# Optimization experiments

Measured on AMD Instinct MI355X. Metric: run time of the kernel, lower is better.

Reference implementation:

```python
import jax, jax.numpy as jnp
import numpy as np

NEG_SLOPE = 0.01  # nn.LeakyReLU default used in module

def leaky_relu(x):
    return jnp.where(x >= 0, x, NEG_SLOPE * x)

def setup_inputs() -> dict:
    key = jax.random.key(0)
    k1, k2, k3, k4, k5 = jax.random.split(key, 5)
    B, S, D, H, E = 4, 2048, 1024, 2048, 8
    s_in = 1.0 / np.sqrt(D)
    return {
        "inputs": jax.random.normal(k1, (B, S, D), dtype=jnp.float32),
        "Wg": jax.random.normal(k2, (E, D), dtype=jnp.float32) * s_in,
        "bg": jax.random.normal(k3, (E,), dtype=jnp.float32) * s_in,
        "We": jax.random.normal(k4, (E, H, D), dtype=jnp.float32) * s_in,
        "be": jax.random.normal(k5, (E, H), dtype=jnp.float32) * s_in,
    }

def reference(inputs, Wg, bg, We, be):
    # gate: [B,S,E]
    gate_logits = jnp.einsum('bsd,ed->bse', inputs, Wg) + bg
    gate_probs = jax.nn.softmax(gate_logits, axis=-1)
    # all experts densely: [B,S,E,H]
    expert_out = leaky_relu(jnp.einsum('bsd,ehd->bseh', inputs, We) + be)
    # gate-weighted reduction over experts: [B,S,H]
    weighted = jnp.einsum('bseh,bse->bsh', expert_out, gate_probs)
    return weighted
```

## Files before the change

kernel.cpp:

```cpp
#include <hip/hip_runtime.h>
#include <hip/hip_bf16.h>
#include <math.h>

#define M_TOK 8192
#define N_H   2048
#define K_D   1024
#define N_E   8

typedef __bf16 bf16x8 __attribute__((ext_vector_type(8)));
typedef __bf16 bf16x4 __attribute__((ext_vector_type(4)));
typedef float  f32x4  __attribute__((ext_vector_type(4)));

__device__ inline f32x4 mfma16(bf16x8 a, bf16x8 b, f32x4 c) {
  return __builtin_amdgcn_mfma_f32_16x16x32_bf16(a, b, c, 0, 0, 0);
}

__device__ inline void load16_lds(const void* g, void* l) {
  __builtin_amdgcn_global_load_lds(
      (const __attribute__((address_space(1))) void*)g,
      (__attribute__((address_space(3))) void*)l, 16, 0, 0);
}

__global__ __launch_bounds__(256) void cvt_kernel(const float* __restrict__ src,
                                                  __bf16* __restrict__ dst,
                                                  int n4) {
  int i = blockIdx.x * blockDim.x + threadIdx.x;
  const int stride = gridDim.x * blockDim.x;
  for (; i < n4; i += stride) {
    float4 v = ((const float4*)src)[i];
    bf16x4 o = {(__bf16)v.x, (__bf16)v.y, (__bf16)v.z, (__bf16)v.w};
    *(bf16x4*)(dst + (size_t)i * 4) = o;
  }
}

__global__ __launch_bounds__(256) void gate_kernel(const float* __restrict__ X,
                                                   const float* __restrict__ Wg,
                                                   const float* __restrict__ bg,
                                                   float* __restrict__ gate,
                                                   __bf16* __restrict__ Xb) {
  const int tid = threadIdx.x;
  const int lane = tid & 63;
  const int wv = tid >> 6;
  const int token = blockIdx.x * 4 + wv;
  const float* xrow = X + (size_t)token * K_D;

  float xr[16];
#pragma unroll
  for (int i = 0; i < 16; ++i) xr[i] = xrow[lane + i * 64];

#pragma unroll
  for (int i = 0; i < 16; ++i)
    Xb[(size_t)token * K_D + lane + i * 64] = (__bf16)xr[i];

  float l[N_E];
#pragma unroll
  for (int e = 0; e < N_E; ++e) {
    const float* wrow = Wg + e * K_D;
    float s = 0.f;
#pragma unroll
    for (int i = 0; i < 16; ++i) s += xr[i] * wrow[lane + i * 64];
#pragma unroll
    for (int off = 32; off > 0; off >>= 1) s += __shfl_xor(s, off);
    l[e] = s + bg[e];
  }
  float mx = l[0];
#pragma unroll
  for (int e = 1; e < N_E; ++e) mx = fmaxf(mx, l[e]);
  float p[N_E], den = 0.f;
#pragma unroll
  for (int e = 0; e < N_E; ++e) { p[e] = expf(l[e] - mx); den += p[e]; }
  const float inv = 1.f / den;
  if (lane == 0) {
#pragma unroll
    for (int e = 0; e < N_E; ++e) gate[(size_t)token * N_E + e] = p[e] * inv;
  }
}

__global__ __launch_bounds__(256, 2) void moe_main(
    const __bf16* __restrict__ Xb, const __bf16* __restrict__ Wb,
    const float* __restrict__ gate, const float* __restrict__ be,
    float* __restrict__ out) {
  __shared__ __bf16 As[2][128 * 32];
  __shared__ __bf16 Bs[2][256 * 32];
  __shared__ float gS[128 * 8];
  __shared__ float bS[8 * 128];

  const int tid = threadIdx.x;
  const int lane = tid & 63;
  const int wv = tid >> 6;
  const int wr = wv >> 1, wn = wv & 1;
  const int row0 = blockIdx.x * 128;
  const int col0 = blockIdx.y * 128;

  for (int i = tid; i < 1024; i += 256) {
    gS[i] = gate[(size_t)row0 * N_E + i];
    bS[i] = be[(size_t)(i >> 7) * N_H + col0 + (i & 127)];
  }

  const int rA = tid >> 2;
  const int kk = (tid & 3) * 8;
  const __bf16* aB = Xb + (size_t)(row0 + rA) * K_D + kk;
  const __bf16* bB = Wb + (size_t)(col0 + rA) * K_D + kk;

  const int lr = lane & 15;
  const int lk = (lane >> 4) * 8;
  const __bf16* aRd0 = &As[0][(wr * 64 + lr) * 32 + lk];
  const __bf16* aRd1 = &As[1][(wr * 64 + lr) * 32 + lk];
  const __bf16* bRd0 = &Bs[0][(wn * 64 + lr) * 32 + lk];
  const __bf16* bRd1 = &Bs[1][(wn * 64 + lr) * 32 + lk];

  f32x4 fin[4][4];
#pragma unroll
  for (int m = 0; m < 4; ++m)
#pragma unroll
    for (int h = 0; h < 4; ++h) fin[m][h] = (f32x4){0.f, 0.f, 0.f, 0.f};

  f32x4 acc[4][8];
#pragma unroll
  for (int m = 0; m < 4; ++m)
#pragma unroll
    for (int n = 0; n < 8; ++n) acc[m][n] = (f32x4){0.f, 0.f, 0.f, 0.f};

  auto STAGE = [&](int tn, int bufN) {
    const int k0 = (tn & 31) << 5;
    const size_t pOff = (size_t)(tn >> 5) << 22;
    const __bf16* a = aB + k0;
    load16_lds(a, &As[bufN][wv * 512]);
    load16_lds(a + (size_t)64 * K_D, &As[bufN][2048 + wv * 512]);
    const __bf16* b = bB + pOff + k0;
    load16_lds(b, &Bs[bufN][wv * 512]);
    load16_lds(b + (size_t)64 * K_D, &Bs[bufN][2048 + wv * 512]);
    load16_lds(b + (size_t)N_H * K_D, &Bs[bufN][4096 + wv * 512]);
    load16_lds(b + (size_t)(N_H + 64) * K_D, &Bs[bufN][6144 + wv * 512]);
  };

  auto EPI = [&](int p) {
    const int e0 = p * 2;
#pragma unroll
    for (int m = 0; m < 4; ++m) {
#pragma unroll
      for (int j = 0; j < 4; ++j) {
        const int r = wr * 64 + m * 16 + (lane >> 4) * 4 + j;
        const float g0 = gS[r * 8 + e0];
        const float g1 = gS[r * 8 + e0 + 1];
#pragma unroll
        for (int h = 0; h < 4; ++h) {
          const int c = wn * 64 + h * 16 + lr;
          float v0 = acc[m][h][j] + bS[e0 * 128 + c];
          v0 = (v0 >= 0.f) ? v0 : 0.01f * v0;
          float v1 = acc[m][4 + h][j] + bS[(e0 + 1) * 128 + c];
          v1 = (v1 >= 0.f) ? v1 : 0.01f * v1;
          fin[m][h][j] += g0 * v0 + g1 * v1;
        }
      }
    }
#pragma unroll
    for (int m = 0; m < 4; ++m)
#pragma unroll
      for (int n = 0; n < 8; ++n) acc[m][n] = (f32x4){0.f, 0.f, 0.f, 0.f};
  };

  auto STEP = [&](int t, const __bf16* aRd, const __bf16* bRd, int nextBuf) {
    if (t < 127) STAGE(t + 1, nextBuf);
    bf16x8 af[4];
#pragma unroll
    for (int m = 0; m < 4; ++m) af[m] = *(const bf16x8*)(aRd + m * 512);
    __builtin_amdgcn_s_setprio(1);
#pragma unroll
    for (int n = 0; n < 8; ++n) {
      const bf16x8 bfr =
          *(const bf16x8*)(bRd + ((n >> 2) * 128 + (n & 3) * 16) * 32);
#pragma unroll
      for (int m = 0; m < 4; ++m)
        acc[m][n] = mfma16(af[m], bfr, acc[m][n]);
    }
    __builtin_amdgcn_s_setprio(0);
    if ((t & 31) == 31) EPI(t >> 5);
    __syncthreads();
  };

  STAGE(0, 0);
  __syncthreads();

#pragma unroll 1
  for (int t2 = 0; t2 < 128; t2 += 2) {
    STEP(t2 + 0, aRd0, bRd0, 1);
    STEP(t2 + 1, aRd1, bRd1, 0);
  }

#pragma unroll
  for (int m = 0; m < 4; ++m) {
#pragma unroll
    for (int j = 0; j < 4; ++j) {
      const size_t r = (size_t)(row0 + wr * 64 + m * 16 + (lane >> 4) * 4 + j);
#pragma unroll
      for (int h = 0; h < 4; ++h) {
        out[r * N_H + col0 + wn * 64 + h * 16 + lr] = fin[m][h][j];
      }
    }
  }
}

extern "C" void kernel_launch(void* const* d_in, const int* in_sizes, int n_in,
                              void* d_out, int out_size, void* d_ws, size_t ws_size,
                              hipStream_t stream) {
  const float* X  = (const float*)d_in[0];
  const float* Wg = (const float*)d_in[1];
  const float* bg = (const float*)d_in[2];
  const float* We = (const float*)d_in[3];
  const float* be = (const float*)d_in[4];
  float* out = (float*)d_out;

  char* ws = (char*)d_ws;
  __bf16* Xb   = (__bf16*)(ws);
  __bf16* Wb   = (__bf16*)(ws + (size_t)16 * 1024 * 1024);
  float*  gate = (float*)(ws + (size_t)48 * 1024 * 1024);

  cvt_kernel<<<2048, 256, 0, stream>>>(We, Wb, (N_E * N_H * K_D) / 4);

  gate_kernel<<<M_TOK / 4, 256, 0, stream>>>(X, Wg, bg, gate, Xb);

  dim3 grid(M_TOK / 128, N_H / 128);
  moe_main<<<grid, 256, 0, stream>>>(Xb, Wb, gate, be, out);
}
```

Measured before the change: 314.2 us.

## Deepen GEMM prefetch to two tiles in flight with explicit vmcnt waits

Restructures the main loop so two K-tiles are in flight instead of one. Each step waits with a manual s_waitcnt vmcnt(6) and a barrier, loads all A and B fragments from LDS into registers, then barriers again. Only after that does it issue the global-to-LDS load for tile t+2 into the buffer it just drained, and finally runs the MFMAs. This is meant to hide more global-memory latency behind compute. The cost is a second barrier per step, more live registers for the B fragments, and a correctness dependence on hand-counted vmcnt values.

```diff
diff --git a/kernel.cpp b/kernel.cpp
--- a/kernel.cpp
+++ b/kernel.cpp
@@ -160,33 +160,47 @@
       for (int n = 0; n < 8; ++n) acc[m][n] = (f32x4){0.f, 0.f, 0.f, 0.f};
   };
 
-  auto STEP = [&](int t, const __bf16* aRd, const __bf16* bRd, int nextBuf) {
-    if (t < 127) STAGE(t + 1, nextBuf);
-    bf16x8 af[4];
+  auto STEP = [&](int t, const __bf16* aRd, const __bf16* bRd, int bufN,
+                  bool doStage, bool lastStep) {
+    if (lastStep)
+      asm volatile("s_waitcnt vmcnt(0)" ::: "memory");
+    else
+      asm volatile("s_waitcnt vmcnt(6)" ::: "memory");
+    __builtin_amdgcn_s_barrier();
+
+    bf16x8 af[4], bfr[8];
 #pragma unroll
     for (int m = 0; m < 4; ++m) af[m] = *(const bf16x8*)(aRd + m * 512);
+#pragma unroll
+    for (int n = 0; n < 8; ++n)
+      bfr[n] = *(const bf16x8*)(bRd + ((n >> 2) * 128 + (n & 3) * 16) * 32);
+    asm volatile("s_waitcnt lgkmcnt(0)" ::: "memory");
+    __builtin_amdgcn_sched_barrier(0);
+    __builtin_amdgcn_s_barrier();
+
+    if (doStage) STAGE(t + 2, bufN);
+
     __builtin_amdgcn_s_setprio(1);
 #pragma unroll
-    for (int n = 0; n < 8; ++n) {
-      const bf16x8 bfr =
-          *(const bf16x8*)(bRd + ((n >> 2) * 128 + (n & 3) * 16) * 32);
+    for (int n = 0; n < 8; ++n)
 #pragma unroll
       for (int m = 0; m < 4; ++m)
-        acc[m][n] = mfma16(af[m], bfr, acc[m][n]);
-    }
+        acc[m][n] = mfma16(af[m], bfr[n], acc[m][n]);
     __builtin_amdgcn_s_setprio(0);
+
     if ((t & 31) == 31) EPI(t >> 5);
-    __syncthreads();
   };
 
   STAGE(0, 0);
-  __syncthreads();
+  STAGE(1, 1);
 
 #pragma unroll 1
-  for (int t2 = 0; t2 < 128; t2 += 2) {
-    STEP(t2 + 0, aRd0, bRd0, 1);
-    STEP(t2 + 1, aRd1, bRd1, 0);
-  }
+  for (int t2 = 0; t2 < 126; t2 += 2) {
+    STEP(t2 + 0, aRd0, bRd0, 0, true, false);
+    STEP(t2 + 1, aRd1, bRd1, 1, true, false);
+  }
+  STEP(126, aRd0, bRd0, 0, false, false);
+  STEP(127, aRd1, bRd1, 1, false, true);
 
 #pragma unroll
   for (int m = 0; m < 4; ++m) {
```

Result: no change. 313.5 us (-0.2%).
